# Optimization experiments

Hardware: AMD Instinct MI355X
Metric: run time of the kernel (lower is better)

## Reference

```python
import jax, jax.numpy as jnp
import numpy as np

B = 1024
HP_ORDER = 4
N_GRID = 72 * (8 ** HP_ORDER)  # 294912 rotations in the SO(3) healpix grid


def _random_rotmats(key, n):
    """Uniform random rotation matrices via normalized quaternions."""
    q = jax.random.normal(key, (n, 4), dtype=jnp.float32)
    q = q / jnp.linalg.norm(q, axis=-1, keepdims=True)
    w, x, y, z = q[:, 0], q[:, 1], q[:, 2], q[:, 3]
    R = jnp.stack([
        jnp.stack([1 - 2 * (y * y + z * z), 2 * (x * y - w * z), 2 * (x * z + w * y)], axis=-1),
        jnp.stack([2 * (x * y + w * z), 1 - 2 * (x * x + z * z), 2 * (y * z - w * x)], axis=-1),
        jnp.stack([2 * (x * z - w * y), 2 * (y * z + w * x), 1 - 2 * (x * x + y * y)], axis=-1),
    ], axis=-2)  # [n, 3, 3]
    return R


def setup_inputs() -> dict:
    key = jax.random.key(0)
    k1, k2 = jax.random.split(key)
    rotMat = _random_rotmats(k1, B)            # [B, 3, 3] query rotations
    output_rotmats = _random_rotmats(k2, N_GRID)  # [N, 3, 3] fixed grid (buffer)
    return {"rotMat": rotMat, "output_rotmats": output_rotmats}


def reference(rotMat, output_rotmats):
    # trace(A @ R_n^T) == sum_ij A_ij * R_n_ij  -> GEMM with K=9
    sim = jnp.einsum('bij,nij->bn', rotMat, output_rotmats)  # [B, N]
    idxs = jnp.argmax(sim, axis=1)                            # [B]
    dot_trace = jnp.max(sim, axis=1)                          # [B]
    nearest = output_rotmats[idxs]                            # [B, 3, 3]
    return dot_trace, nearest
```

## Files before the change

### kernel.cpp

```cpp
#include <hip/hip_runtime.h>

#define B_TOTAL 1024
#define NGRID   294912
#define NTILES  (NGRID / 16)
#define MARGIN  6e-4f
#define CAP     (1u << 20)

#define NBLK2   512
#define TPB     (NTILES / NBLK2)
#define TPW2    (TPB / 4)

#define KEYS_OFF   0u
#define WSMAX_OFF  8192u
#define CNT_OFF    12288u
#define CAND_OFF   16384u
#define APACK_OFF  4210688u
#define GPACK_OFF  4276224u
#define WS_NEED    23150592u

typedef __attribute__((ext_vector_type(8))) short short8v;
typedef __attribute__((ext_vector_type(4))) float float4v;

__device__ __forceinline__ unsigned short f2bf(float x) {
    unsigned u = __float_as_uint(x);
    unsigned r = ((u >> 16) & 1u) + 0x7FFFu;
    return (unsigned short)((u + r) >> 16);
}
__device__ __forceinline__ float bf2f(unsigned short b) {
    return __uint_as_float(((unsigned)b) << 16);
}
__device__ __forceinline__ unsigned ford(float f) {
    unsigned u = __float_as_uint(f);
    return (u & 0x80000000u) ? ~u : (u | 0x80000000u);
}
__device__ __forceinline__ float funord(unsigned u) {
    return __uint_as_float((u & 0x80000000u) ? (u & 0x7FFFFFFFu) : ~u);
}

__global__ __launch_bounds__(256)
void so3_init_kernel(unsigned long long* __restrict__ keys,
                     unsigned* __restrict__ wsmax, unsigned* __restrict__ cnt) {
    int i = blockIdx.x * 256 + threadIdx.x;
    if (i < B_TOTAL) { keys[i] = 0ull; wsmax[i] = 0u; }
    if (i == 0) *cnt = 0u;
}

__global__ __launch_bounds__(256)
void so3_pack_kernel(const float* __restrict__ src, unsigned* __restrict__ dst,
                     int nrows, int isA) {
    int id = blockIdx.x * 256 + threadIdx.x;
    if (id >= nrows * 16) return;
    int r = id >> 4, i = id & 15;
    unsigned w = 0;
    #pragma unroll
    for (int h = 0; h < 2; ++h) {
        int s = i * 2 + h;
        unsigned short v = 0;
        if (s < 27) {
            int k = (s < 9) ? s : (s < 18 ? s - 9 : s - 18);
            float x = src[(size_t)r * 9 + k];
            unsigned short hi = f2bf(x);
            int wantLo = isA ? (s >= 18) : (s >= 9 && s < 18);
            v = wantLo ? f2bf(x - bf2f(hi)) : hi;
        }
        w |= ((unsigned)v) << (16 * h);
    }
    dst[id] = w;
}

__device__ __forceinline__ void stage_A(const unsigned short* __restrict__ Ap,
                                        unsigned short* sB, int t) {
    #pragma unroll
    for (int i = 0; i < 16; ++i) {
        int id = t + i * 256;
        int row = id >> 2, kb = id & 3;
        uint4 v = *(const uint4*)(Ap + row * 32 + kb * 8);
        int skb = kb ^ ((row >> 1) & 3);
        *(uint4*)((char*)sB + row * 64 + skb * 16) = v;
    }
}

__global__ __launch_bounds__(256, 2)
void so3_mfma_max_kernel(const unsigned short* __restrict__ Ap,
                         const unsigned short* __restrict__ Gp,
                         unsigned* __restrict__ wsmax) {
    __shared__ __align__(16) unsigned short sB[1024 * 32];
    __shared__ float sW[4][64][16];
    const int t = threadIdx.x, l = t & 63, w = t >> 6;
    const int lr = l & 15, lk = l >> 4;

    stage_A(Ap, sB, t);

    const int tile0 = blockIdx.x * TPB + w * TPW2;
    short8v af[TPW2];
    #pragma unroll
    for (int i = 0; i < TPW2; ++i)
        af[i] = *(const short8v*)(Gp + (size_t)((tile0 + i) * 16 + lr) * 32 + lk * 8);

    __syncthreads();

    for (int qt = 0; qt < 64; ++qt) {
        const int row = qt * 16 + lr;
        const int skb = lk ^ ((row >> 1) & 3);
        short8v bf = *(const short8v*)((const char*)sB + row * 64 + skb * 16);
        float m = -1e30f;
        #pragma unroll
        for (int i = 0; i < TPW2; ++i) {
            float4v c = {0.f, 0.f, 0.f, 0.f};
            c = __builtin_amdgcn_mfma_f32_16x16x32_bf16(af[i], bf, c, 0, 0, 0);
            float m3 = fmaxf(fmaxf(c[0], c[1]), c[2]);
            m = fmaxf(fmaxf(m3, c[3]), m);
        }
        m = fmaxf(m, __shfl_xor(m, 16));
        m = fmaxf(m, __shfl_xor(m, 32));
        if (l < 16) sW[w][qt][l] = m;
    }
    __syncthreads();

    for (int e = t; e < 1024; e += 256) {
        int qt = e >> 4, q = e & 15;
        float v = fmaxf(fmaxf(sW[0][qt][q], sW[1][qt][q]),
                        fmaxf(sW[2][qt][q], sW[3][qt][q]));
        unsigned u = ford(v);
        unsigned* p = wsmax + e;
        if (u > *p) atomicMax(p, u);
    }
}

__global__ __launch_bounds__(256, 2)
void so3_mfma_cand_kernel(const unsigned short* __restrict__ Ap,
                          const unsigned short* __restrict__ Gp,
                          const unsigned* __restrict__ wsmax,
                          unsigned* __restrict__ cnt,
                          unsigned* __restrict__ cands) {
    __shared__ __align__(16) unsigned short sB[1024 * 32];
    __shared__ float sThr[1024];
    const int t = threadIdx.x, l = t & 63, w = t >> 6;
    const int lr = l & 15, lk = l >> 4;

    stage_A(Ap, sB, t);
    for (int e = t; e < 1024; e += 256)
        sThr[e] = funord(wsmax[e]) - MARGIN;

    const int tile0 = blockIdx.x * TPB + w * TPW2;
    short8v af[TPW2];
    #pragma unroll
    for (int i = 0; i < TPW2; ++i)
        af[i] = *(const short8v*)(Gp + (size_t)((tile0 + i) * 16 + lr) * 32 + lk * 8);

    __syncthreads();

    for (int qt = 0; qt < 64; ++qt) {
        const int row = qt * 16 + lr;
        const float thr = sThr[row];
        const int skb = lk ^ ((row >> 1) & 3);
        short8v bf = *(const short8v*)((const char*)sB + row * 64 + skb * 16);
        #pragma unroll
        for (int i = 0; i < TPW2; ++i) {
            float4v c = {0.f, 0.f, 0.f, 0.f};
            c = __builtin_amdgcn_mfma_f32_16x16x32_bf16(af[i], bf, c, 0, 0, 0);
            float m4 = fmaxf(fmaxf(fmaxf(c[0], c[1]), c[2]), c[3]);
            if (m4 >= thr) {
                #pragma unroll
                for (int r = 0; r < 4; ++r) {
                    if (c[r] >= thr) {
                        int n = (tile0 + i) * 16 + lk * 4 + r;
                        unsigned idx = atomicAdd(cnt, 1u);
                        if (idx < CAP)
                            cands[idx] = ((unsigned)row << 19) | (unsigned)n;
                    }
                }
            }
        }
    }
}

__global__ __launch_bounds__(256)
void so3_rescore_kernel(const float* __restrict__ A, const float* __restrict__ G,
                        const unsigned* __restrict__ cnt,
                        const unsigned* __restrict__ cands,
                        unsigned long long* __restrict__ keys) {
    unsigned total = *cnt;
    if (total > CAP) total = CAP;
    const unsigned stride = gridDim.x * 256;
    for (unsigned i = blockIdx.x * 256 + threadIdx.x; i < total; i += stride) {
        unsigned cd = cands[i];
        int b = (int)(cd >> 19), n = (int)(cd & 0x7FFFFu);
        const float* a = A + (size_t)b * 9;
        const float* g = G + (size_t)n * 9;
        float d;
        d = a[0] * g[0];
        d = fmaf(a[1], g[1], d);
        d = fmaf(a[2], g[2], d);
        d = fmaf(a[3], g[3], d);
        d = fmaf(a[4], g[4], d);
        d = fmaf(a[5], g[5], d);
        d = fmaf(a[6], g[6], d);
        d = fmaf(a[7], g[7], d);
        d = fmaf(a[8], g[8], d);
        unsigned long long key =
            ((unsigned long long)ford(d) << 32) | (unsigned)(~n);
        unsigned long long seen = keys[b];
        if (key > seen) atomicMax(&keys[b], key);
    }
}

__global__ __launch_bounds__(256)
void so3_final_kernel(const float* __restrict__ G,
                      const unsigned long long* __restrict__ keys,
                      float* __restrict__ out) {
    int b = blockIdx.x * 256 + threadIdx.x;
    if (b >= B_TOTAL) return;
    unsigned long long key = keys[b];
    unsigned hi = (unsigned)(key >> 32);
    int idx = (int)(~(unsigned)key);
    out[b] = funord(hi);
    const float* g = G + (size_t)idx * 9;
    float* o = out + B_TOTAL + (size_t)b * 9;
    #pragma unroll
    for (int k = 0; k < 9; ++k) o[k] = g[k];
}

#define FB_NBLK  2048
#define FB_CHUNK (NGRID / FB_NBLK)
#define FB_NTHR  128
#define FB_BPT   8
__global__ __launch_bounds__(FB_NTHR, 4)
void so3_fb_partial_kernel(const float* __restrict__ A, const float* __restrict__ G,
                           unsigned long long* __restrict__ ws) {
    __shared__ __align__(16) float sG[FB_CHUNK * 12];
    const int t = threadIdx.x;
    const int n0 = blockIdx.x * FB_CHUNK;
    for (int i = t; i < FB_CHUNK * 9; i += FB_NTHR) {
        int row = i / 9, k = i - row * 9;
        sG[row * 12 + k] = G[(size_t)n0 * 9 + i];
    }
    float a[FB_BPT][9];
    #pragma unroll
    for (int j = 0; j < FB_BPT; ++j) {
        const float* ap = A + (size_t)(j * FB_NTHR + t) * 9;
        #pragma unroll
        for (int k = 0; k < 9; ++k) a[j][k] = ap[k];
    }
    float best[FB_BPT]; int bidx[FB_BPT];
    #pragma unroll
    for (int j = 0; j < FB_BPT; ++j) { best[j] = -1e30f; bidx[j] = 0; }
    __syncthreads();
    #pragma unroll 2
    for (int n = 0; n < FB_CHUNK; ++n) {
        const float4* gv = (const float4*)(sG + n * 12);
        const float4 gA = gv[0], gB = gv[1];
        const float g8 = sG[n * 12 + 8];
        const int vn = n0 + n;
        #pragma unroll
        for (int j = 0; j < FB_BPT; ++j) {
            float d;
            d = a[j][0] * gA.x; d = fmaf(a[j][1], gA.y, d); d = fmaf(a[j][2], gA.z, d);
            d = fmaf(a[j][3], gA.w, d); d = fmaf(a[j][4], gB.x, d); d = fmaf(a[j][5], gB.y, d);
            d = fmaf(a[j][6], gB.z, d); d = fmaf(a[j][7], gB.w, d); d = fmaf(a[j][8], g8, d);
            if (d > best[j]) { best[j] = d; bidx[j] = vn; }
        }
    }
    #pragma unroll
    for (int j = 0; j < FB_BPT; ++j) {
        unsigned long long key =
            ((unsigned long long)ford(best[j]) << 32) | (unsigned)(~bidx[j]);
        unsigned long long seen = ws[j * FB_NTHR + t];
        if (key > seen) atomicMax(&ws[j * FB_NTHR + t], key);
    }
}

extern "C" void kernel_launch(void* const* d_in, const int* in_sizes, int n_in,
                              void* d_out, int out_size, void* d_ws, size_t ws_size,
                              hipStream_t stream) {
    const float* A = (const float*)d_in[0];
    const float* G = (const float*)d_in[1];
    float* out = (float*)d_out;
    char* ws = (char*)d_ws;
    unsigned long long* keys = (unsigned long long*)(ws + KEYS_OFF);
    unsigned* wsmax = (unsigned*)(ws + WSMAX_OFF);
    unsigned* cnt   = (unsigned*)(ws + CNT_OFF);
    unsigned* cands = (unsigned*)(ws + CAND_OFF);
    unsigned short* Ap = (unsigned short*)(ws + APACK_OFF);
    unsigned short* Gp = (unsigned short*)(ws + GPACK_OFF);

    if (ws_size < WS_NEED) {
        hipLaunchKernelGGL(so3_init_kernel, dim3(4), dim3(256), 0, stream,
                           keys, wsmax, cnt);
        hipLaunchKernelGGL(so3_fb_partial_kernel, dim3(FB_NBLK), dim3(FB_NTHR),
                           0, stream, A, G, keys);
        hipLaunchKernelGGL(so3_final_kernel, dim3(4), dim3(256), 0, stream,
                           G, keys, out);
        return;
    }

    hipLaunchKernelGGL(so3_init_kernel, dim3(4), dim3(256), 0, stream,
                       keys, wsmax, cnt);
    hipLaunchKernelGGL(so3_pack_kernel, dim3((B_TOTAL * 16) / 256), dim3(256),
                       0, stream, A, (unsigned*)Ap, B_TOTAL, 1);
    hipLaunchKernelGGL(so3_pack_kernel, dim3((NGRID * 16) / 256), dim3(256),
                       0, stream, G, (unsigned*)Gp, NGRID, 0);
    hipLaunchKernelGGL(so3_mfma_max_kernel, dim3(NBLK2), dim3(256), 0, stream,
                       Ap, Gp, wsmax);
    hipLaunchKernelGGL(so3_mfma_cand_kernel, dim3(NBLK2), dim3(256), 0, stream,
                       Ap, Gp, wsmax, cnt, cands);
    hipLaunchKernelGGL(so3_rescore_kernel, dim3(128), dim3(256), 0, stream,
                       A, G, cnt, cands, keys);
    hipLaunchKernelGGL(so3_final_kernel, dim3(4), dim3(256), 0, stream,
                       G, keys, out);
}
```

Baseline: 103.2 us.

## Split query batch across a second grid dimension and drop shuffle reductions

```diff
diff --git a/kernel.cpp b/kernel.cpp
--- a/kernel.cpp
+++ b/kernel.cpp
@@ -6,8 +6,10 @@
 #define MARGIN  6e-4f
 #define CAP     (1u << 20)
 
-#define NBLK2   512
-#define TPB     (NTILES / NBLK2)
+#define QBLK    256
+#define QTILES  (QBLK / 16)
+#define NSLICE  512
+#define TPB     (NTILES / NSLICE)
 #define TPW2    (TPB / 4)
 
 #define KEYS_OFF   0u
@@ -69,27 +71,35 @@
 }
 
 __device__ __forceinline__ void stage_A(const unsigned short* __restrict__ Ap,
-                                        unsigned short* sB, int t) {
-    #pragma unroll
-    for (int i = 0; i < 16; ++i) {
+                                        unsigned short* sB, int t, int qbase) {
+    #pragma unroll
+    for (int i = 0; i < QBLK / 64; ++i) {
         int id = t + i * 256;
         int row = id >> 2, kb = id & 3;
-        uint4 v = *(const uint4*)(Ap + row * 32 + kb * 8);
+        uint4 v = *(const uint4*)(Ap + (size_t)(qbase + row) * 32 + kb * 8);
         int skb = kb ^ ((row >> 1) & 3);
         *(uint4*)((char*)sB + row * 64 + skb * 16) = v;
     }
 }
 
-__global__ __launch_bounds__(256, 2)
+__device__ __forceinline__ float tree_max9(const float* m4) {
+    float a = fmaxf(fmaxf(m4[0], m4[1]), m4[2]);
+    float b = fmaxf(fmaxf(m4[3], m4[4]), m4[5]);
+    float c = fmaxf(fmaxf(m4[6], m4[7]), m4[8]);
+    return fmaxf(fmaxf(a, b), c);
+}
+
+__global__ __launch_bounds__(256, 4)
 void so3_mfma_max_kernel(const unsigned short* __restrict__ Ap,
                          const unsigned short* __restrict__ Gp,
                          unsigned* __restrict__ wsmax) {
-    __shared__ __align__(16) unsigned short sB[1024 * 32];
-    __shared__ float sW[4][64][16];
+    __shared__ __align__(16) unsigned short sB[QBLK * 32];
+    __shared__ float sW[4][QTILES][4][16];
     const int t = threadIdx.x, l = t & 63, w = t >> 6;
     const int lr = l & 15, lk = l >> 4;
-
-    stage_A(Ap, sB, t);
+    const int qbase = blockIdx.y * QBLK;
+
+    stage_A(Ap, sB, t, qbase);
 
     const int tile0 = blockIdx.x * TPB + w * TPW2;
     short8v af[TPW2];
@@ -99,48 +109,50 @@
 
     __syncthreads();
 
-    for (int qt = 0; qt < 64; ++qt) {
+    for (int qt = 0; qt < QTILES; ++qt) {
         const int row = qt * 16 + lr;
         const int skb = lk ^ ((row >> 1) & 3);
         short8v bf = *(const short8v*)((const char*)sB + row * 64 + skb * 16);
-        float m = -1e30f;
+        float m4[TPW2];
         #pragma unroll
         for (int i = 0; i < TPW2; ++i) {
             float4v c = {0.f, 0.f, 0.f, 0.f};
             c = __builtin_amdgcn_mfma_f32_16x16x32_bf16(af[i], bf, c, 0, 0, 0);
-            float m3 = fmaxf(fmaxf(c[0], c[1]), c[2]);
-            m = fmaxf(fmaxf(m3, c[3]), m);
+            m4[i] = fmaxf(fmaxf(c[0], c[1]), fmaxf(c[2], c[3]));
         }
-        m = fmaxf(m, __shfl_xor(m, 16));
-        m = fmaxf(m, __shfl_xor(m, 32));
-        if (l < 16) sW[w][qt][l] = m;
+        sW[w][qt][lk][lr] = tree_max9(m4);
     }
     __syncthreads();
 
-    for (int e = t; e < 1024; e += 256) {
+    {
+        int e = t;
         int qt = e >> 4, q = e & 15;
-        float v = fmaxf(fmaxf(sW[0][qt][q], sW[1][qt][q]),
-                        fmaxf(sW[2][qt][q], sW[3][qt][q]));
+        float v = -1e30f;
+        #pragma unroll
+        for (int ww = 0; ww < 4; ++ww)
+            #pragma unroll
+            for (int kk = 0; kk < 4; ++kk)
+                v = fmaxf(v, sW[ww][qt][kk][q]);
         unsigned u = ford(v);
-        unsigned* p = wsmax + e;
+        unsigned* p = wsmax + qbase + e;
         if (u > *p) atomicMax(p, u);
     }
 }
 
-__global__ __launch_bounds__(256, 2)
+__global__ __launch_bounds__(256, 4)
 void so3_mfma_cand_kernel(const unsigned short* __restrict__ Ap,
                           const unsigned short* __restrict__ Gp,
                           const unsigned* __restrict__ wsmax,
                           unsigned* __restrict__ cnt,
                           unsigned* __restrict__ cands) {
-    __shared__ __align__(16) unsigned short sB[1024 * 32];
-    __shared__ float sThr[1024];
+    __shared__ __align__(16) unsigned short sB[QBLK * 32];
+    __shared__ float sThr[QBLK];
     const int t = threadIdx.x, l = t & 63, w = t >> 6;
     const int lr = l & 15, lk = l >> 4;
-
-    stage_A(Ap, sB, t);
-    for (int e = t; e < 1024; e += 256)
-        sThr[e] = funord(wsmax[e]) - MARGIN;
+    const int qbase = blockIdx.y * QBLK;
+
+    stage_A(Ap, sB, t, qbase);
+    sThr[t] = funord(wsmax[qbase + t]) - MARGIN;
 
     const int tile0 = blockIdx.x * TPB + w * TPW2;
     short8v af[TPW2];
@@ -150,7 +162,7 @@
 
     __syncthreads();
 
-    for (int qt = 0; qt < 64; ++qt) {
+    for (int qt = 0; qt < QTILES; ++qt) {
         const int row = qt * 16 + lr;
         const float thr = sThr[row];
         const int skb = lk ^ ((row >> 1) & 3);
@@ -159,15 +171,16 @@
         for (int i = 0; i < TPW2; ++i) {
             float4v c = {0.f, 0.f, 0.f, 0.f};
             c = __builtin_amdgcn_mfma_f32_16x16x32_bf16(af[i], bf, c, 0, 0, 0);
-            float m4 = fmaxf(fmaxf(fmaxf(c[0], c[1]), c[2]), c[3]);
+            float m4 = fmaxf(fmaxf(c[0], c[1]), fmaxf(c[2], c[3]));
             if (m4 >= thr) {
+                int b = qbase + row;
                 #pragma unroll
                 for (int r = 0; r < 4; ++r) {
                     if (c[r] >= thr) {
                         int n = (tile0 + i) * 16 + lk * 4 + r;
                         unsigned idx = atomicAdd(cnt, 1u);
                         if (idx < CAP)
-                            cands[idx] = ((unsigned)row << 19) | (unsigned)n;
+                            cands[idx] = ((unsigned)b << 19) | (unsigned)n;
                     }
                 }
             }
@@ -300,10 +313,10 @@
                        0, stream, A, (unsigned*)Ap, B_TOTAL, 1);
     hipLaunchKernelGGL(so3_pack_kernel, dim3((NGRID * 16) / 256), dim3(256),
                        0, stream, G, (unsigned*)Gp, NGRID, 0);
-    hipLaunchKernelGGL(so3_mfma_max_kernel, dim3(NBLK2), dim3(256), 0, stream,
-                       Ap, Gp, wsmax);
-    hipLaunchKernelGGL(so3_mfma_cand_kernel, dim3(NBLK2), dim3(256), 0, stream,
-                       Ap, Gp, wsmax, cnt, cands);
+    hipLaunchKernelGGL(so3_mfma_max_kernel, dim3(NSLICE, B_TOTAL / QBLK),
+                       dim3(256), 0, stream, Ap, Gp, wsmax);
+    hipLaunchKernelGGL(so3_mfma_cand_kernel, dim3(NSLICE, B_TOTAL / QBLK),
+                       dim3(256), 0, stream, Ap, Gp, wsmax, cnt, cands);
     hipLaunchKernelGGL(so3_rescore_kernel, dim3(128), dim3(256), 0, stream,
                        A, G, cnt, cands, keys);
     hipLaunchKernelGGL(so3_final_kernel, dim3(4), dim3(256), 0, stream,
```

After: 87.90 us. -14.8%, faster.
